# Kernel optimization log

Measured on AMD Instinct MI355X. Metric: run time of the kernel, lower is better.

## Reference

```python
import jax, jax.numpy as jnp
import numpy as np


def setup_inputs() -> dict:
    key = jax.random.key(0)
    k1, k2 = jax.random.split(key)
    in_features, out_features, tokens = 4096, 4096, 8192
    x = jax.random.normal(k1, (tokens, in_features), dtype=jnp.float32)
    bound = 1.0 / np.sqrt(in_features)  # nn.Linear default init -> |W| <= 1
    W = jax.random.uniform(k2, (out_features, in_features), dtype=jnp.float32,
                           minval=-bound, maxval=bound)
    return {"x": x, "W": W}


def reference(x, W):
    # Forward of BinarizedLinear: y = x @ sign(W)^T (bias-free linear with
    # sign-binarized weights; the clamp_(-1,1) after sign() is a no-op).
    Wb = jnp.sign(W)  # [out, in], values in {-1, 0, +1}
    return jnp.einsum('ti,oi->to', x, Wb)  # [tokens, out]
```

## Files before the change

### kernel.cpp

```cpp
#include <hip/hip_runtime.h>
#include <hip/hip_bf16.h>
#include <stdint.h>

#define M_TOK 8192
#define N_OUT 4096
#define K_IN  4096

#define BM 256
#define BN 256
#define BKB 128
#define NT (K_IN / BKB)

typedef __attribute__((ext_vector_type(4))) int   i32x4;
typedef __attribute__((ext_vector_type(4))) float f32x4;

#define AS1 __attribute__((address_space(1)))
#define AS3 __attribute__((address_space(3)))
#define GLOAD_LDS16(g, l) \
  __builtin_amdgcn_global_load_lds((AS1 void*)(g), (AS3 void*)(l), 16, 0, 0)

#define BAR()     __builtin_amdgcn_s_barrier()
#define WAITALL() asm volatile("s_waitcnt vmcnt(0) lgkmcnt(0)" ::: "memory")
#define VMCNT8()  asm volatile("s_waitcnt vmcnt(8)" ::: "memory")
#define LGKM12()  asm volatile("s_waitcnt lgkmcnt(12)" ::: "memory")
#define SCHEDB()  __builtin_amdgcn_sched_barrier(0)
#define PRIO(p)   __builtin_amdgcn_s_setprio(p)
#define MFMAI8(a, b, c) __builtin_amdgcn_mfma_i32_16x16x64_i8((a), (b), (c), 0, 0, 0)

__global__ __launch_bounds__(256) void quant_x_i8(const float4* __restrict__ x,
                                                  int4* __restrict__ o,
                                                  float* __restrict__ scales) {
  const int row = blockIdx.x;
  const int t   = threadIdx.x;
  const float4* xr = x + (size_t)row * (K_IN / 4);
  float4 v[4];
  #pragma unroll
  for (int i = 0; i < 4; ++i) v[i] = xr[t * 4 + i];
  float m = 0.f;
  #pragma unroll
  for (int i = 0; i < 4; ++i)
    m = fmaxf(m, fmaxf(fmaxf(fabsf(v[i].x), fabsf(v[i].y)),
                       fmaxf(fabsf(v[i].z), fabsf(v[i].w))));
  #pragma unroll
  for (int off = 32; off; off >>= 1) m = fmaxf(m, __shfl_down(m, off));
  __shared__ float sm[4];
  if ((t & 63) == 0) sm[t >> 6] = m;
  __syncthreads();
  m = fmaxf(fmaxf(sm[0], sm[1]), fmaxf(sm[2], sm[3]));
  const float inv = m > 0.f ? 127.f / m : 0.f;
  if (t == 0) scales[row] = m > 0.f ? m / 127.f : 1.f;
  int q[4];
  #pragma unroll
  for (int i = 0; i < 4; ++i) {
    const int a0 = (int)rintf(v[i].x * inv);
    const int a1 = (int)rintf(v[i].y * inv);
    const int a2 = (int)rintf(v[i].z * inv);
    const int a3 = (int)rintf(v[i].w * inv);
    q[i] = (a0 & 255) | ((a1 & 255) << 8) | ((a2 & 255) << 16) | (a3 << 24);
  }
  o[(size_t)row * (K_IN / 16) + t] = make_int4(q[0], q[1], q[2], q[3]);
}

__global__ __launch_bounds__(256) void sgn_w_i8(const float4* __restrict__ w,
                                                int4* __restrict__ o, int n16) {
  int i = blockIdx.x * blockDim.x + threadIdx.x;
  int stride = gridDim.x * blockDim.x;
  for (; i < n16; i += stride) {
    int q[4];
    #pragma unroll
    for (int j = 0; j < 4; ++j) {
      float4 v = w[i * 4 + j];
      const int a0 = v.x > 0.f ? 1 : (v.x < 0.f ? -1 : 0);
      const int a1 = v.y > 0.f ? 1 : (v.y < 0.f ? -1 : 0);
      const int a2 = v.z > 0.f ? 1 : (v.z < 0.f ? -1 : 0);
      const int a3 = v.w > 0.f ? 1 : (v.w < 0.f ? -1 : 0);
      q[j] = (a0 & 255) | ((a1 & 255) << 8) | ((a2 & 255) << 16) | (a3 << 24);
    }
    o[i] = make_int4(q[0], q[1], q[2], q[3]);
  }
}

__global__ __launch_bounds__(512, 2) void bin_gemm_i8(const char* __restrict__ A,
                                                      const char* __restrict__ B,
                                                      const float* __restrict__ scales,
                                                      float* __restrict__ C) {
  __shared__ char lds[131072];

  const int tid  = threadIdx.x;
  const int w    = tid >> 6;
  const int lane = tid & 63;
  const int lr   = lane & 15;
  const int lk   = lane >> 4;
  const int wr   = w >> 2;
  const int wc   = w & 3;

  const int bm = blockIdx.x >> 4;
  const int bn = blockIdx.x & 15;

  const char* Ag = A + (size_t)bm * BM * K_IN;
  const char* Bg = B + (size_t)bn * BN * K_IN;

  const int c0 = w * 128 + lane;
  const int c1 = c0 + 64;
  const int r0 = c0 >> 3, r1 = c1 >> 3;
  const size_t g0 = (size_t)r0 * K_IN + (size_t)(((c0 ^ r0) & 7) << 4);
  const size_t g1 = (size_t)r1 * K_IN + (size_t)(((c1 ^ r1) & 7) << 4);
  const int ldsw = w * 128 * 16;

  auto stage = [&](int mat, int half, int tt) {
    const char* g = (mat ? Bg : Ag) + (size_t)half * (128 * K_IN)
                                    + (size_t)tt * BKB;
    char* l = &lds[((tt & 1) << 16) + (mat << 15) + (half << 14) + ldsw];
    GLOAD_LDS16(g + g0, l);
    GLOAD_LDS16(g + g1, l + 1024);
  };

  const int swz   = (lr & 7) << 4;
  const int a_row = (wr * 128 + lr) * 128;
  const int b_row = 32768 + (wc * 64 + lr) * 128;
  const int k0 = (lk * 16) ^ swz;
  const int k1 = (64 + lk * 16) ^ swz;

  i32x4 acc[8][4];
  #pragma unroll
  for (int m = 0; m < 8; ++m)
    #pragma unroll
    for (int n = 0; n < 4; ++n) { i32x4 z = {0, 0, 0, 0}; acc[m][n] = z; }

  i32x4 aA[8], bA[4], aB[8], bB[4];

  stage(0, 0, 0); stage(0, 1, 0); stage(1, 0, 0); stage(1, 1, 0);
  stage(0, 0, 1); stage(0, 1, 1); stage(1, 0, 1); stage(1, 1, 1);
  VMCNT8();
  BAR();
  {
    const char* L0 = &lds[0];
    #pragma unroll
    for (int m = 0; m < 8; ++m) aA[m] = *(const i32x4*)(L0 + a_row + m * 2048 + k0);
    #pragma unroll
    for (int n = 0; n < 4; ++n) bA[n] = *(const i32x4*)(L0 + b_row + n * 2048 + k0);
  }

  for (int t = 0; t < NT; ++t) {
    const char* Lc = &lds[(size_t)(t & 1) << 16];
    const char* Ln = &lds[(size_t)(~t & 1) << 16];

    #pragma unroll
    for (int m = 0; m < 8; ++m) aB[m] = *(const i32x4*)(Lc + a_row + m * 2048 + k1);
    #pragma unroll
    for (int n = 0; n < 4; ++n) bB[n] = *(const i32x4*)(Lc + b_row + n * 2048 + k1);
    LGKM12();
    SCHEDB();
    PRIO(1);
    #pragma unroll
    for (int m = 0; m < 8; ++m)
      #pragma unroll
      for (int n = 0; n < 4; ++n)
        acc[m][n] = MFMAI8(aA[m], bA[n], acc[m][n]);
    PRIO(0);

    WAITALL();
    BAR();

    if (t + 2 < NT) {
      stage(1, 0, t + 2); stage(1, 1, t + 2);
      stage(0, 0, t + 2); stage(0, 1, t + 2);
    }
    if (t + 1 < NT) {
      #pragma unroll
      for (int m = 0; m < 8; ++m) aA[m] = *(const i32x4*)(Ln + a_row + m * 2048 + k0);
      #pragma unroll
      for (int n = 0; n < 4; ++n) bA[n] = *(const i32x4*)(Ln + b_row + n * 2048 + k0);
    }
    SCHEDB();
    PRIO(1);
    #pragma unroll
    for (int m = 0; m < 8; ++m)
      #pragma unroll
      for (int n = 0; n < 4; ++n)
        acc[m][n] = MFMAI8(aB[m], bB[n], acc[m][n]);
    PRIO(0);
  }

  const int grow0 = bm * BM + wr * 128;
  float scl[8][4];
  #pragma unroll
  for (int m = 0; m < 8; ++m)
    #pragma unroll
    for (int j = 0; j < 4; ++j)
      scl[m][j] = scales[grow0 + m * 16 + lk * 4 + j];

  float* Cp = C + (size_t)grow0 * N_OUT + bn * BN + wc * 64;
  #pragma unroll
  for (int m = 0; m < 8; ++m)
    #pragma unroll
    for (int n = 0; n < 4; ++n)
      #pragma unroll
      for (int j = 0; j < 4; ++j)
        Cp[(size_t)(m * 16 + lk * 4 + j) * N_OUT + n * 16 + lr] =
            (float)acc[m][n][j] * scl[m][j];
}

__global__ __launch_bounds__(256) void fb_gemm(const float* __restrict__ x,
                                               const float* __restrict__ W,
                                               float* __restrict__ y) {
  __shared__ float xs[32][33];
  __shared__ float ws[32][33];
  const int bx = blockIdx.x;
  const int by = blockIdx.y;
  const int tx = threadIdx.x & 31;
  const int ty = threadIdx.x >> 5;
  float acc[4] = {0.f, 0.f, 0.f, 0.f};
  for (int k0 = 0; k0 < K_IN; k0 += 32) {
    #pragma unroll
    for (int i = 0; i < 4; ++i) {
      int r = ty + i * 8;
      xs[r][tx] = x[(size_t)(by * 32 + r) * K_IN + k0 + tx];
      float wv = W[(size_t)(bx * 32 + r) * K_IN + k0 + tx];
      ws[r][tx] = wv > 0.f ? 1.f : (wv < 0.f ? -1.f : 0.f);
    }
    __syncthreads();
    #pragma unroll
    for (int i = 0; i < 4; ++i) {
      int r = ty + i * 8;
      float s = acc[i];
      #pragma unroll
      for (int k = 0; k < 32; ++k) s += xs[r][k] * ws[tx][k];
      acc[i] = s;
    }
    __syncthreads();
  }
  #pragma unroll
  for (int i = 0; i < 4; ++i)
    y[(size_t)(by * 32 + ty + i * 8) * N_OUT + bx * 32 + tx] = acc[i];
}

extern "C" void kernel_launch(void* const* d_in, const int* in_sizes, int n_in,
                              void* d_out, int out_size, void* d_ws, size_t ws_size,
                              hipStream_t stream) {
  const float* x = (const float*)d_in[0];
  const float* W = (const float*)d_in[1];
  float* y = (float*)d_out;

  const size_t need = (size_t)M_TOK * K_IN + (size_t)N_OUT * K_IN
                    + (size_t)M_TOK * sizeof(float);
  if (ws_size >= need) {
    char*  xq = (char*)d_ws;
    char*  wq = xq + (size_t)M_TOK * K_IN;
    float* sc = (float*)(wq + (size_t)N_OUT * K_IN);
    quant_x_i8<<<M_TOK, 256, 0, stream>>>((const float4*)x, (int4*)xq, sc);
    sgn_w_i8<<<2048, 256, 0, stream>>>((const float4*)W, (int4*)wq,
                                       N_OUT * K_IN / 16);
    bin_gemm_i8<<<(M_TOK / BM) * (N_OUT / BN), 512, 0, stream>>>(xq, wq, sc, y);
  } else {
    dim3 g(N_OUT / 32, M_TOK / 32);
    fb_gemm<<<g, 256, 0, stream>>>(x, W, y);
  }
}
```

Measured before the change: 180.2 us.

## Load B fragments directly from global into registers, halve LDS footprint

The int8 GEMM no longer stages the sign-weight tile B through LDS. Each wave reads its B fragments straight from global memory into registers, while only A is double-buffered in LDS (64 KB instead of 128 KB). The main loop is unrolled by two with a hand-placed vmcnt/barrier schedule that interleaves global B loads with the MFMA blocks. This cuts LDS traffic and footprint, which may allow more occupancy. In exchange it relies on uncoalesced per-lane global B reads hitting in cache, and on fragile vmcnt counting that mixes the LDS-DMA and register loads.

```diff
diff --git a/kernel.cpp b/kernel.cpp
--- a/kernel.cpp
+++ b/kernel.cpp
@@ -12,19 +12,16 @@
 #define NT (K_IN / BKB)
 
 typedef __attribute__((ext_vector_type(4))) int   i32x4;
-typedef __attribute__((ext_vector_type(4))) float f32x4;
 
 #define AS1 __attribute__((address_space(1)))
 #define AS3 __attribute__((address_space(3)))
 #define GLOAD_LDS16(g, l) \
   __builtin_amdgcn_global_load_lds((AS1 void*)(g), (AS3 void*)(l), 16, 0, 0)
 
-#define BAR()     __builtin_amdgcn_s_barrier()
-#define WAITALL() asm volatile("s_waitcnt vmcnt(0) lgkmcnt(0)" ::: "memory")
-#define VMCNT8()  asm volatile("s_waitcnt vmcnt(8)" ::: "memory")
-#define LGKM12()  asm volatile("s_waitcnt lgkmcnt(12)" ::: "memory")
-#define SCHEDB()  __builtin_amdgcn_sched_barrier(0)
-#define PRIO(p)   __builtin_amdgcn_s_setprio(p)
+#define BAR()      __builtin_amdgcn_s_barrier()
+#define VMCNT4()   asm volatile("s_waitcnt vmcnt(4)" ::: "memory")
+#define VMCNT8()   asm volatile("s_waitcnt vmcnt(8)" ::: "memory")
+#define PRIO(p)    __builtin_amdgcn_s_setprio(p)
 #define MFMAI8(a, b, c) __builtin_amdgcn_mfma_i32_16x16x64_i8((a), (b), (c), 0, 0, 0)
 
 __global__ __launch_bounds__(256) void quant_x_i8(const float4* __restrict__ x,
@@ -84,7 +81,7 @@
                                                       const char* __restrict__ B,
                                                       const float* __restrict__ scales,
                                                       float* __restrict__ C) {
-  __shared__ char lds[131072];
+  __shared__ char lds[65536];
 
   const int tid  = threadIdx.x;
   const int w    = tid >> 6;
@@ -105,81 +102,92 @@
   const int r0 = c0 >> 3, r1 = c1 >> 3;
   const size_t g0 = (size_t)r0 * K_IN + (size_t)(((c0 ^ r0) & 7) << 4);
   const size_t g1 = (size_t)r1 * K_IN + (size_t)(((c1 ^ r1) & 7) << 4);
-  const int ldsw = w * 128 * 16;
-
-  auto stage = [&](int mat, int half, int tt) {
-    const char* g = (mat ? Bg : Ag) + (size_t)half * (128 * K_IN)
-                                    + (size_t)tt * BKB;
-    char* l = &lds[((tt & 1) << 16) + (mat << 15) + (half << 14) + ldsw];
+  const int ldsw = w * 2048;
+
+  auto stageA = [&](int half, int tt) {
+    const char* g = Ag + (size_t)half * (128 * K_IN) + (size_t)tt * BKB;
+    char* l = &lds[((tt & 1) << 15) + (half << 14) + ldsw];
     GLOAD_LDS16(g + g0, l);
     GLOAD_LDS16(g + g1, l + 1024);
   };
 
   const int swz   = (lr & 7) << 4;
   const int a_row = (wr * 128 + lr) * 128;
-  const int b_row = 32768 + (wc * 64 + lr) * 128;
   const int k0 = (lk * 16) ^ swz;
   const int k1 = (64 + lk * 16) ^ swz;
 
+  const char* Bw = Bg + (size_t)(wc * 64 + lr) * K_IN + lk * 16;
+  auto loadB = [&](i32x4* dst, int tt, int ks) {
+    #pragma unroll
+    for (int n = 0; n < 4; ++n)
+      dst[n] = *(const i32x4*)(Bw + (size_t)n * 16 * K_IN
+                                  + (size_t)tt * BKB + ks * 64);
+  };
+
   i32x4 acc[8][4];
   #pragma unroll
   for (int m = 0; m < 8; ++m)
     #pragma unroll
     for (int n = 0; n < 4; ++n) { i32x4 z = {0, 0, 0, 0}; acc[m][n] = z; }
 
-  i32x4 aA[8], bA[4], aB[8], bB[4];
-
-  stage(0, 0, 0); stage(0, 1, 0); stage(1, 0, 0); stage(1, 1, 0);
-  stage(0, 0, 1); stage(0, 1, 1); stage(1, 0, 1); stage(1, 1, 1);
-  VMCNT8();
+  i32x4 aH[8], b1[4], bE0[4], bO0[4];
+
+  stageA(0, 0); stageA(1, 0);
+  loadB(bE0, 0, 0);
+  VMCNT4();
   BAR();
-  {
-    const char* L0 = &lds[0];
-    #pragma unroll
-    for (int m = 0; m < 8; ++m) aA[m] = *(const i32x4*)(L0 + a_row + m * 2048 + k0);
-    #pragma unroll
-    for (int n = 0; n < 4; ++n) bA[n] = *(const i32x4*)(L0 + b_row + n * 2048 + k0);
-  }
-
-  for (int t = 0; t < NT; ++t) {
-    const char* Lc = &lds[(size_t)(t & 1) << 16];
-    const char* Ln = &lds[(size_t)(~t & 1) << 16];
-
-    #pragma unroll
-    for (int m = 0; m < 8; ++m) aB[m] = *(const i32x4*)(Lc + a_row + m * 2048 + k1);
-    #pragma unroll
-    for (int n = 0; n < 4; ++n) bB[n] = *(const i32x4*)(Lc + b_row + n * 2048 + k1);
-    LGKM12();
-    SCHEDB();
-    PRIO(1);
-    #pragma unroll
-    for (int m = 0; m < 8; ++m)
-      #pragma unroll
-      for (int n = 0; n < 4; ++n)
-        acc[m][n] = MFMAI8(aA[m], bA[n], acc[m][n]);
-    PRIO(0);
-
-    WAITALL();
+
+  for (int t = 0; t < NT; t += 2) {
+    const char* Le = &lds[0];
+    const char* Lo = &lds[32768];
+
+    stageA(0, t + 1); stageA(1, t + 1);
+    loadB(b1, t, 1);
+    #pragma unroll
+    for (int m = 0; m < 8; ++m) aH[m] = *(const i32x4*)(Le + a_row + m * 2048 + k0);
+    PRIO(1);
+    #pragma unroll
+    for (int q = 0; q < 4; ++q)
+      #pragma unroll
+      for (int m = 0; m < 8; ++m)
+        acc[m][q] = MFMAI8(aH[m], bE0[q], acc[m][q]);
+    PRIO(0);
+    loadB(bO0, t + 1, 0);
+    #pragma unroll
+    for (int m = 0; m < 8; ++m) aH[m] = *(const i32x4*)(Le + a_row + m * 2048 + k1);
+    PRIO(1);
+    #pragma unroll
+    for (int q = 0; q < 4; ++q)
+      #pragma unroll
+      for (int m = 0; m < 8; ++m)
+        acc[m][q] = MFMAI8(aH[m], b1[q], acc[m][q]);
+    PRIO(0);
+    VMCNT8();
     BAR();
 
-    if (t + 2 < NT) {
-      stage(1, 0, t + 2); stage(1, 1, t + 2);
-      stage(0, 0, t + 2); stage(0, 1, t + 2);
-    }
-    if (t + 1 < NT) {
-      #pragma unroll
-      for (int m = 0; m < 8; ++m) aA[m] = *(const i32x4*)(Ln + a_row + m * 2048 + k0);
-      #pragma unroll
-      for (int n = 0; n < 4; ++n) bA[n] = *(const i32x4*)(Ln + b_row + n * 2048 + k0);
-    }
-    SCHEDB();
-    PRIO(1);
-    #pragma unroll
-    for (int m = 0; m < 8; ++m)
-      #pragma unroll
-      for (int n = 0; n < 4; ++n)
-        acc[m][n] = MFMAI8(aB[m], bB[n], acc[m][n]);
-    PRIO(0);
+    if (t + 2 < NT) { stageA(0, t + 2); stageA(1, t + 2); }
+    loadB(b1, t + 1, 1);
+    #pragma unroll
+    for (int m = 0; m < 8; ++m) aH[m] = *(const i32x4*)(Lo + a_row + m * 2048 + k0);
+    PRIO(1);
+    #pragma unroll
+    for (int q = 0; q < 4; ++q)
+      #pragma unroll
+      for (int m = 0; m < 8; ++m)
+        acc[m][q] = MFMAI8(aH[m], bO0[q], acc[m][q]);
+    PRIO(0);
+    if (t + 2 < NT) loadB(bE0, t + 2, 0);
+    #pragma unroll
+    for (int m = 0; m < 8; ++m) aH[m] = *(const i32x4*)(Lo + a_row + m * 2048 + k1);
+    PRIO(1);
+    #pragma unroll
+    for (int q = 0; q < 4; ++q)
+      #pragma unroll
+      for (int m = 0; m < 8; ++m)
+        acc[m][q] = MFMAI8(aH[m], b1[q], acc[m][q]);
+    PRIO(0);
+    VMCNT8();
+    BAR();
   }
 
   const int grow0 = bm * BM + wr * 128;
```

Measured after the change: 291.9 us. +62.0%, slower.

## Shrink int8 GEMM block tile to 256x128x64 with 256 threads

Applied to the files above, without the earlier changes.

Reshapes the binarized int8 GEMM block tile from 256x256 with a K step of 128 and 512 threads to 256x128 with a K step of 64 and 256 threads. LDS use drops from 128KB to 48KB, the LDS swizzle is reworked for 64-byte rows, and the grid doubles in block count. The register-level double buffering of MFMA fragments is dropped: each step loads all fragments once and splits the MFMAs into two halves around the barrier and the next global-to-LDS stage. The aim is higher occupancy and better load balance, at the cost of less data reuse per block and more barriers per unit of work.

```diff
diff --git a/kernel.cpp b/kernel.cpp
--- a/kernel.cpp
+++ b/kernel.cpp
@@ -7,12 +7,11 @@
 #define K_IN  4096
 
 #define BM 256
-#define BN 256
-#define BKB 128
+#define BN 128
+#define BKB 64
 #define NT (K_IN / BKB)
 
-typedef __attribute__((ext_vector_type(4))) int   i32x4;
-typedef __attribute__((ext_vector_type(4))) float f32x4;
+typedef __attribute__((ext_vector_type(4))) int i32x4;
 
 #define AS1 __attribute__((address_space(1)))
 #define AS3 __attribute__((address_space(3)))
@@ -21,9 +20,7 @@
 
 #define BAR()     __builtin_amdgcn_s_barrier()
 #define WAITALL() asm volatile("s_waitcnt vmcnt(0) lgkmcnt(0)" ::: "memory")
-#define VMCNT8()  asm volatile("s_waitcnt vmcnt(8)" ::: "memory")
-#define LGKM12()  asm volatile("s_waitcnt lgkmcnt(12)" ::: "memory")
-#define SCHEDB()  __builtin_amdgcn_sched_barrier(0)
+#define VMCNT6()  asm volatile("s_waitcnt vmcnt(6)" ::: "memory")
 #define PRIO(p)   __builtin_amdgcn_s_setprio(p)
 #define MFMAI8(a, b, c) __builtin_amdgcn_mfma_i32_16x16x64_i8((a), (b), (c), 0, 0, 0)
 
@@ -80,46 +77,56 @@
   }
 }
 
-__global__ __launch_bounds__(512, 2) void bin_gemm_i8(const char* __restrict__ A,
+__global__ __launch_bounds__(256, 2) void bin_gemm_i8(const char* __restrict__ A,
                                                       const char* __restrict__ B,
                                                       const float* __restrict__ scales,
                                                       float* __restrict__ C) {
-  __shared__ char lds[131072];
+  __shared__ char lds[49152];
 
   const int tid  = threadIdx.x;
   const int w    = tid >> 6;
   const int lane = tid & 63;
   const int lr   = lane & 15;
   const int lk   = lane >> 4;
-  const int wr   = w >> 2;
-  const int wc   = w & 3;
-
-  const int bm = blockIdx.x >> 4;
-  const int bn = blockIdx.x & 15;
+  const int wr   = w >> 1;
+  const int wc   = w & 1;
+
+  const int bm = blockIdx.x >> 5;
+  const int bn = blockIdx.x & 31;
 
   const char* Ag = A + (size_t)bm * BM * K_IN;
   const char* Bg = B + (size_t)bn * BN * K_IN;
 
-  const int c0 = w * 128 + lane;
-  const int c1 = c0 + 64;
-  const int r0 = c0 >> 3, r1 = c1 >> 3;
-  const size_t g0 = (size_t)r0 * K_IN + (size_t)(((c0 ^ r0) & 7) << 4);
-  const size_t g1 = (size_t)r1 * K_IN + (size_t)(((c1 ^ r1) & 7) << 4);
-  const int ldsw = w * 128 * 16;
-
-  auto stage = [&](int mat, int half, int tt) {
-    const char* g = (mat ? Bg : Ag) + (size_t)half * (128 * K_IN)
-                                    + (size_t)tt * BKB;
-    char* l = &lds[((tt & 1) << 16) + (mat << 15) + (half << 14) + ldsw];
-    GLOAD_LDS16(g + g0, l);
-    GLOAD_LDS16(g + g1, l + 1024);
+  const int ca0 = w * 256 + lane;
+  const int cb0 = w * 128 + lane;
+  size_t gA[4], gB[2];
+  #pragma unroll
+  for (int j = 0; j < 4; ++j) {
+    const int c = ca0 + j * 64;
+    const int r = c >> 2;
+    gA[j] = (size_t)r * K_IN + (size_t)((((c & 3) ^ ((r >> 1) & 3))) << 4);
+  }
+  #pragma unroll
+  for (int j = 0; j < 2; ++j) {
+    const int c = cb0 + j * 64;
+    const int r = c >> 2;
+    gB[j] = (size_t)r * K_IN + (size_t)((((c & 3) ^ ((r >> 1) & 3))) << 4);
+  }
+
+  auto stage = [&](int tt) {
+    const size_t koff = (size_t)tt * BKB;
+    char* base = &lds[(tt & 1) * 24576];
+    #pragma unroll
+    for (int j = 0; j < 4; ++j)
+      GLOAD_LDS16(Ag + gA[j] + koff, base + w * 4096 + j * 1024);
+    #pragma unroll
+    for (int j = 0; j < 2; ++j)
+      GLOAD_LDS16(Bg + gB[j] + koff, base + 16384 + w * 2048 + j * 1024);
   };
 
-  const int swz   = (lr & 7) << 4;
-  const int a_row = (wr * 128 + lr) * 128;
-  const int b_row = 32768 + (wc * 64 + lr) * 128;
-  const int k0 = (lk * 16) ^ swz;
-  const int k1 = (64 + lk * 16) ^ swz;
+  const int kof   = (lk ^ ((lr >> 1) & 3)) << 4;
+  const int a_row = (wr * 128 + lr) * 64;
+  const int b_row = 16384 + (wc * 64 + lr) * 64;
 
   i32x4 acc[8][4];
   #pragma unroll
@@ -127,58 +134,39 @@
     #pragma unroll
     for (int n = 0; n < 4; ++n) { i32x4 z = {0, 0, 0, 0}; acc[m][n] = z; }
 
-  i32x4 aA[8], bA[4], aB[8], bB[4];
-
-  stage(0, 0, 0); stage(0, 1, 0); stage(1, 0, 0); stage(1, 1, 0);
-  stage(0, 0, 1); stage(0, 1, 1); stage(1, 0, 1); stage(1, 1, 1);
-  VMCNT8();
+  stage(0);
+  stage(1);
+  VMCNT6();
   BAR();
-  {
-    const char* L0 = &lds[0];
-    #pragma unroll
-    for (int m = 0; m < 8; ++m) aA[m] = *(const i32x4*)(L0 + a_row + m * 2048 + k0);
-    #pragma unroll
-    for (int n = 0; n < 4; ++n) bA[n] = *(const i32x4*)(L0 + b_row + n * 2048 + k0);
-  }
 
   for (int t = 0; t < NT; ++t) {
-    const char* Lc = &lds[(size_t)(t & 1) << 16];
-    const char* Ln = &lds[(size_t)(~t & 1) << 16];
-
-    #pragma unroll
-    for (int m = 0; m < 8; ++m) aB[m] = *(const i32x4*)(Lc + a_row + m * 2048 + k1);
-    #pragma unroll
-    for (int n = 0; n < 4; ++n) bB[n] = *(const i32x4*)(Lc + b_row + n * 2048 + k1);
-    LGKM12();
-    SCHEDB();
+    const char* L = &lds[(t & 1) * 24576];
+    i32x4 aF[8], bF[4];
+
+    #pragma unroll
+    for (int m = 0; m < 8; ++m)
+      aF[m] = *(const i32x4*)(L + a_row + m * 1024 + kof);
+    #pragma unroll
+    for (int n = 0; n < 4; ++n)
+      bF[n] = *(const i32x4*)(L + b_row + n * 1024 + kof);
     PRIO(1);
     #pragma unroll
-    for (int m = 0; m < 8; ++m)
+    for (int m = 0; m < 4; ++m)
       #pragma unroll
       for (int n = 0; n < 4; ++n)
-        acc[m][n] = MFMAI8(aA[m], bA[n], acc[m][n]);
+        acc[m][n] = MFMAI8(aF[m], bF[n], acc[m][n]);
     PRIO(0);
 
     WAITALL();
     BAR();
 
-    if (t + 2 < NT) {
-      stage(1, 0, t + 2); stage(1, 1, t + 2);
-      stage(0, 0, t + 2); stage(0, 1, t + 2);
-    }
-    if (t + 1 < NT) {
-      #pragma unroll
-      for (int m = 0; m < 8; ++m) aA[m] = *(const i32x4*)(Ln + a_row + m * 2048 + k0);
-      #pragma unroll
-      for (int n = 0; n < 4; ++n) bA[n] = *(const i32x4*)(Ln + b_row + n * 2048 + k0);
-    }
-    SCHEDB();
+    if (t + 2 < NT) stage(t + 2);
     PRIO(1);
     #pragma unroll
-    for (int m = 0; m < 8; ++m)
+    for (int m = 4; m < 8; ++m)
       #pragma unroll
       for (int n = 0; n < 4; ++n)
-        acc[m][n] = MFMAI8(aB[m], bB[n], acc[m][n]);
+        acc[m][n] = MFMAI8(aF[m], bF[n], acc[m][n]);
     PRIO(0);
   }
 
@@ -251,7 +239,7 @@
     quant_x_i8<<<M_TOK, 256, 0, stream>>>((const float4*)x, (int4*)xq, sc);
     sgn_w_i8<<<2048, 256, 0, stream>>>((const float4*)W, (int4*)wq,
                                        N_OUT * K_IN / 16);
-    bin_gemm_i8<<<(M_TOK / BM) * (N_OUT / BN), 512, 0, stream>>>(xq, wq, sc, y);
+    bin_gemm_i8<<<(M_TOK / BM) * (N_OUT / BN), 256, 0, stream>>>(xq, wq, sc, y);
   } else {
     dim3 g(N_OUT / 32, M_TOK / 32);
     fb_gemm<<<g, 256, 0, stream>>>(x, W, y);
```

Result: slower. 196.2 us (+8.9%).
